# Kernel optimization log

Hardware: AMD Instinct MI355X
Metric: run time of the kernel (lower is better)

Reference implementation:

```python
import jax, jax.numpy as jnp
import numpy as np

K = 8        # number of nearest neighbors (idw default)
POWER = 2    # inverse-distance power (idw default)
EPS = 1e-8


def setup_inputs() -> dict:
    key = jax.random.key(0)
    kq, kr, kf = jax.random.split(key, 3)
    N, M = 32768, 16384
    # scale coords so points are spread out like real LiDAR scenes
    query_points = jax.random.normal(kq, (N, 3), dtype=jnp.float32) * 10.0
    ref_points = jax.random.normal(kr, (M, 3), dtype=jnp.float32) * 10.0
    ref_flow = jax.random.normal(kf, (M, 3), dtype=jnp.float32)
    return {"query_points": query_points, "ref_points": ref_points, "ref_flow": ref_flow}


def reference(query_points, ref_points, ref_flow):
    # cdist: Euclidean distance [N, M] via (q-r)^2 = |q|^2 + |r|^2 - 2 q.r
    q2 = jnp.sum(query_points * query_points, axis=-1, keepdims=True)      # [N,1]
    r2 = jnp.sum(ref_points * ref_points, axis=-1)                          # [M]
    d2 = q2 + r2 - 2.0 * (query_points @ ref_points.T)                      # [N,M]
    dist = jnp.sqrt(jnp.maximum(d2, 0.0))
    # k smallest distances == top_k of negated distances
    neg_knn, knn_idx = jax.lax.top_k(-dist, K)                               # [N,K]
    knn_dist = -neg_knn
    # inverse-distance weights: 1 / (d^power + eps), normalized over k
    weights = 1.0 / (knn_dist ** POWER + EPS)
    weights = weights / jnp.sum(weights, axis=1, keepdims=True)
    knn_flow = ref_flow[knn_idx]                                             # [N,K,3]
    return jnp.sum(weights[..., None] * knn_flow, axis=1)                    # [N,3]
```

## Files before the change

kernel.cpp:

```cpp
#include <hip/hip_runtime.h>

#define KNN    8
#define BLOCK  256
#define TILE   2048
#define GD     32
#define NC     (GD*GD*GD)
#define EPSW   1e-8f
#define BIGF   3.4e38f

__device__ __forceinline__ void insert8(float d2, int j, float bd[KNN], int bi[KNN]) {
    if (d2 < bd[0]) {
        bd[0] = d2; bi[0] = j;
#pragma unroll
        for (int t = 0; t < KNN - 1; t++) {
            if (bd[t] < bd[t + 1]) {
                float td = bd[t]; bd[t] = bd[t + 1]; bd[t + 1] = td;
                int   ti = bi[t]; bi[t] = bi[t + 1]; bi[t + 1] = ti;
            }
        }
    }
}

__device__ __forceinline__ void ced(float& a, int& ai, float& b, int& bi) {
    if (a < b) { float t = a; a = b; b = t; int ti = ai; ai = bi; bi = ti; }
}
__device__ __forceinline__ void sort8_desc(float d[KNN], int ix[KNN]) {
    ced(d[0],ix[0],d[4],ix[4]); ced(d[1],ix[1],d[5],ix[5]);
    ced(d[2],ix[2],d[6],ix[6]); ced(d[3],ix[3],d[7],ix[7]);
    ced(d[0],ix[0],d[2],ix[2]); ced(d[1],ix[1],d[3],ix[3]);
    ced(d[4],ix[4],d[6],ix[6]); ced(d[5],ix[5],d[7],ix[7]);
    ced(d[0],ix[0],d[1],ix[1]); ced(d[2],ix[2],d[3],ix[3]);
    ced(d[4],ix[4],d[5],ix[5]); ced(d[6],ix[6],d[7],ix[7]);
}
__device__ __forceinline__ void merge_lists(float bd[KNN], int bi[KNN], int mask, bool sort_after) {
    float pd[KNN]; int pi[KNN];
#pragma unroll
    for (int j = 0; j < KNN; j++) { pd[j] = __shfl_xor(bd[j], mask); pi[j] = __shfl_xor(bi[j], mask); }
#pragma unroll
    for (int j = 0; j < KNN; j++) {
        if (pd[KNN - 1 - j] < bd[j]) { bd[j] = pd[KNN - 1 - j]; bi[j] = pi[KNN - 1 - j]; }
    }
    if (sort_after) sort8_desc(bd, bi);
}
__device__ __forceinline__ float merged_thr4(const float bd[KNN]) {
    float c[KNN], p[KNN];
#pragma unroll
    for (int j = 0; j < KNN; j++) c[j] = bd[j];
#pragma unroll
    for (int j = 0; j < KNN; j++) p[j] = __shfl_xor(c[j], 1);
#pragma unroll
    for (int j = 0; j < KNN; j++) c[j] = fminf(c[j], p[KNN - 1 - j]);
    {
        float mx, mn;
        mx = fmaxf(c[0],c[4]); mn = fminf(c[0],c[4]); c[0]=mx; c[4]=mn;
        mx = fmaxf(c[1],c[5]); mn = fminf(c[1],c[5]); c[1]=mx; c[5]=mn;
        mx = fmaxf(c[2],c[6]); mn = fminf(c[2],c[6]); c[2]=mx; c[6]=mn;
        mx = fmaxf(c[3],c[7]); mn = fminf(c[3],c[7]); c[3]=mx; c[7]=mn;
        mx = fmaxf(c[0],c[2]); mn = fminf(c[0],c[2]); c[0]=mx; c[2]=mn;
        mx = fmaxf(c[1],c[3]); mn = fminf(c[1],c[3]); c[1]=mx; c[3]=mn;
        mx = fmaxf(c[4],c[6]); mn = fminf(c[4],c[6]); c[4]=mx; c[6]=mn;
        mx = fmaxf(c[5],c[7]); mn = fminf(c[5],c[7]); c[5]=mx; c[7]=mn;
        mx = fmaxf(c[0],c[1]); mn = fminf(c[0],c[1]); c[0]=mx; c[1]=mn;
        mx = fmaxf(c[2],c[3]); mn = fminf(c[2],c[3]); c[2]=mx; c[3]=mn;
        mx = fmaxf(c[4],c[5]); mn = fminf(c[4],c[5]); c[4]=mx; c[5]=mn;
        mx = fmaxf(c[6],c[7]); mn = fminf(c[6],c[7]); c[6]=mx; c[7]=mn;
    }
#pragma unroll
    for (int j = 0; j < KNN; j++) p[j] = __shfl_xor(c[j], 2);
#pragma unroll
    for (int j = 0; j < KNN; j++) c[j] = fminf(c[j], p[KNN - 1 - j]);
    float m = c[0];
#pragma unroll
    for (int j = 1; j < KNN; j++) m = fmaxf(m, c[j]);
    return m;
}

__device__ __forceinline__ unsigned fenc(float f) {
    unsigned u = __float_as_uint(f);
    return (u & 0x80000000u) ? ~u : (u | 0x80000000u);
}
__device__ __forceinline__ float fdec(unsigned e) {
    unsigned u = (e & 0x80000000u) ? (e ^ 0x80000000u) : ~e;
    return __uint_as_float(u);
}

__device__ __forceinline__ void load_bb(const unsigned* __restrict__ bbw,
                                        float mn[3], float inv[3], float& hmin) {
    hmin = BIGF;
#pragma unroll
    for (int a = 0; a < 3; a++) {
        float lo = fdec(bbw[a]), hi = -fdec(bbw[3 + a]);
        float w = fmaxf(hi - lo, 1e-9f);
        mn[a] = lo;
        inv[a] = (float)GD / w;
        hmin = fminf(hmin, w / (float)GD);
    }
}

__device__ __forceinline__ int cell_clamp(int c) {
    return c < 0 ? 0 : (c > GD - 1 ? GD - 1 : c);
}


__global__ __launch_bounds__(256) void bbox_zero(const float* __restrict__ r, int M,
                                                 unsigned* __restrict__ bbw,
                                                 int* __restrict__ zbase, int zcount) {
    int idx = blockIdx.x * 256 + threadIdx.x;
    for (int j = idx; j < zcount; j += gridDim.x * 256) zbase[j] = 0;
    float mn0 = BIGF, mn1 = BIGF, mn2 = BIGF;
    float mx0 = -BIGF, mx1 = -BIGF, mx2 = -BIGF;
    for (int j = idx; j < M; j += gridDim.x * 256) {
        float x = r[3 * j], y = r[3 * j + 1], z = r[3 * j + 2];
        mn0 = fminf(mn0, x); mx0 = fmaxf(mx0, x);
        mn1 = fminf(mn1, y); mx1 = fmaxf(mx1, y);
        mn2 = fminf(mn2, z); mx2 = fmaxf(mx2, z);
    }
#pragma unroll
    for (int o = 32; o > 0; o >>= 1) {
        mn0 = fminf(mn0, __shfl_xor(mn0, o));
        mn1 = fminf(mn1, __shfl_xor(mn1, o));
        mn2 = fminf(mn2, __shfl_xor(mn2, o));
        mx0 = fmaxf(mx0, __shfl_xor(mx0, o));
        mx1 = fmaxf(mx1, __shfl_xor(mx1, o));
        mx2 = fmaxf(mx2, __shfl_xor(mx2, o));
    }
    if ((threadIdx.x & 63) == 0) {
        atomicMin(bbw + 0, fenc(mn0)); atomicMin(bbw + 1, fenc(mn1)); atomicMin(bbw + 2, fenc(mn2));
        atomicMin(bbw + 3, fenc(-mx0)); atomicMin(bbw + 4, fenc(-mx1)); atomicMin(bbw + 5, fenc(-mx2));
    }
}

__global__ __launch_bounds__(256) void hist2(const float* __restrict__ r,
                                             const float* __restrict__ q,
                                             int M, int N, const unsigned* __restrict__ bbw,
                                             int* __restrict__ rcid, int* __restrict__ qcid,
                                             int* __restrict__ rcnt, int* __restrict__ qcnt) {
    float mn[3], inv[3], hmin;
    load_bb(bbw, mn, inv, hmin);
    int i = blockIdx.x * 256 + threadIdx.x;
    if (i < M) {
        int cx = cell_clamp((int)((r[3 * i]     - mn[0]) * inv[0]));
        int cy = cell_clamp((int)((r[3 * i + 1] - mn[1]) * inv[1]));
        int cz = cell_clamp((int)((r[3 * i + 2] - mn[2]) * inv[2]));
        int cid = (cz * GD + cy) * GD + cx;
        rcid[i] = cid;
        atomicAdd(rcnt + cid, 1);
    } else if (i < M + N) {
        int j = i - M;
        int cx = cell_clamp((int)((q[3 * j]     - mn[0]) * inv[0]));
        int cy = cell_clamp((int)((q[3 * j + 1] - mn[1]) * inv[1]));
        int cz = cell_clamp((int)((q[3 * j + 2] - mn[2]) * inv[2]));
        int cid = (cz * GD + cy) * GD + cx;
        qcid[j] = cid;
        atomicAdd(qcnt + cid, 1);
    }
}

__global__ __launch_bounds__(1024) void scan2(int* __restrict__ rcnt, int* __restrict__ rstart,
                                              int* __restrict__ qcnt, int* __restrict__ qstart) {
    int* cnt = (blockIdx.x == 0) ? rcnt : qcnt;
    int* st  = (blockIdx.x == 0) ? rstart : qstart;
    __shared__ int part[1024];
    int t = threadIdx.x;
    int base = t * 32;
    int s = 0;
#pragma unroll
    for (int k = 0; k < 32; k++) s += cnt[base + k];
    part[t] = s;
    __syncthreads();
    for (int off = 1; off < 1024; off <<= 1) {
        int v = (t >= off) ? part[t - off] : 0;
        __syncthreads();
        part[t] += v;
        __syncthreads();
    }
    int run = part[t] - s;
#pragma unroll
    for (int k = 0; k < 32; k++) {
        int c = cnt[base + k];
        st[base + k] = run;
        cnt[base + k] = run;
        run += c;
    }
    if (t == 1023) st[NC] = run;
}

__global__ __launch_bounds__(256) void scatter2(const float* __restrict__ r, int M, int N,
                                                const int* __restrict__ rcid,
                                                const int* __restrict__ qcid,
                                                int* __restrict__ rcur, int* __restrict__ qcur,
                                                float4* __restrict__ rps, int* __restrict__ sidx,
                                                int* __restrict__ qorder) {
    int i = blockIdx.x * 256 + threadIdx.x;
    if (i < M) {
        int pos = atomicAdd(rcur + rcid[i], 1);
        float x = r[3 * i], y = r[3 * i + 1], z = r[3 * i + 2];
        rps[pos] = make_float4(x, y, z, x * x + y * y + z * z);
        sidx[pos] = i;
    } else if (i < M + N) {
        int j = i - M;
        int pos = atomicAdd(qcur + qcid[j], 1);
        qorder[pos] = j;
    }
}

__device__ __forceinline__ void scan_shell(
    int R, int cx, int cy, int cz, int sub,
    const float4* __restrict__ rps, const int* __restrict__ rstart,
    float qx, float qy, float qz, float q2,
    float bd[KNN], int bi[KNN], float& thr) {
    for (int dz = -R; dz <= R; ++dz) {
        int z = cz + dz;
        if ((unsigned)z >= GD) continue;
        for (int dy = -R; dy <= R; ++dy) {
            int y = cy + dy;
            if ((unsigned)y >= GD) continue;
            int rowb = (z * GD + y) * GD;
            if (dz == -R || dz == R || dy == -R || dy == R) {
                int x0 = max(cx - R, 0), x1 = min(cx + R, GD - 1);
                int s = rstart[rowb + x0], e = rstart[rowb + x1 + 1];
                for (int ii = s + sub; ii < e; ii += 4) {
                    float4 p = rps[ii];
                    float d2 = (q2 + p.w) - 2.0f * (qx * p.x + qy * p.y + qz * p.z);
                    if (d2 < thr) { insert8(d2, ii, bd, bi); thr = bd[0]; }
                }
            } else {
                int xl = cx - R, xr = cx + R;
                if (xl >= 0) {
                    int s = rstart[rowb + xl], e = rstart[rowb + xl + 1];
                    for (int ii = s + sub; ii < e; ii += 4) {
                        float4 p = rps[ii];
                        float d2 = (q2 + p.w) - 2.0f * (qx * p.x + qy * p.y + qz * p.z);
                        if (d2 < thr) { insert8(d2, ii, bd, bi); thr = bd[0]; }
                    }
                }
                if (xr < GD) {
                    int s = rstart[rowb + xr], e = rstart[rowb + xr + 1];
                    for (int ii = s + sub; ii < e; ii += 4) {
                        float4 p = rps[ii];
                        float d2 = (q2 + p.w) - 2.0f * (qx * p.x + qy * p.y + qz * p.z);
                        if (d2 < thr) { insert8(d2, ii, bd, bi); thr = bd[0]; }
                    }
                }
            }
        }
    }
}

__global__ __launch_bounds__(256) void knn_pass1(
    const float4* __restrict__ rps, const int* __restrict__ rstart,
    const int* __restrict__ qorder, const float* __restrict__ q,
    const int* __restrict__ sidx, const float* __restrict__ f,
    const unsigned* __restrict__ bbw, float* __restrict__ out,
    int* __restrict__ pend, int* __restrict__ pcnt, int N) {
    int t = blockIdx.x * 256 + threadIdx.x;
    int g = t >> 2;
    int sub = t & 3;
    if (g >= N) return;
    int qi = qorder[g];
    float qx = q[3 * qi], qy = q[3 * qi + 1], qz = q[3 * qi + 2];
    float q2 = qx * qx + qy * qy + qz * qz;
    float mn[3], inv[3], hmin;
    load_bb(bbw, mn, inv, hmin);
    int cx = cell_clamp((int)((qx - mn[0]) * inv[0]));
    int cy = cell_clamp((int)((qy - mn[1]) * inv[1]));
    int cz = cell_clamp((int)((qz - mn[2]) * inv[2]));

    float bd[KNN]; int bi[KNN];
#pragma unroll
    for (int k = 0; k < KNN; k++) { bd[k] = BIGF; bi[k] = 0; }
    float thr = BIGF;

    int rs[9], re[9];
#pragma unroll
    for (int dz = -1; dz <= 1; dz++) {
#pragma unroll
        for (int dy = -1; dy <= 1; dy++) {
            int k = (dz + 1) * 3 + (dy + 1);
            int z = cz + dz, y = cy + dy;
            if ((unsigned)z >= GD || (unsigned)y >= GD) { rs[k] = 0; re[k] = 0; }
            else {
                int rowb = (z * GD + y) * GD;
                int x0 = max(cx - 1, 0), x1 = min(cx + 1, GD - 1);
                rs[k] = rstart[rowb + x0]; re[k] = rstart[rowb + x1 + 1];
            }
        }
    }
#pragma unroll
    for (int k = 0; k < 9; k++) {
        for (int ii = rs[k] + sub; ii < re[k]; ii += 4) {
            float4 p = rps[ii];
            float d2 = (q2 + p.w) - 2.0f * (qx * p.x + qy * p.y + qz * p.z);
            if (d2 < thr) { insert8(d2, ii, bd, bi); thr = bd[0]; }
        }
    }
    float mthr = merged_thr4(bd);
    thr = fminf(thr, mthr);
    bool done = (mthr <= hmin * hmin);

    if (!done) {
        scan_shell(2, cx, cy, cz, sub, rps, rstart, qx, qy, qz, q2, bd, bi, thr);
        mthr = merged_thr4(bd);
        thr = fminf(thr, mthr);
        done = (mthr <= 4.0f * hmin * hmin);
    }
    if (!done) {
        scan_shell(3, cx, cy, cz, sub, rps, rstart, qx, qy, qz, q2, bd, bi, thr);
        mthr = merged_thr4(bd);
        done = (mthr <= 9.0f * hmin * hmin);
    }

    if (!done) {
        if (sub == 0) { int pos = atomicAdd(pcnt, 1); pend[pos] = qi; }
        return;
    }

    merge_lists(bd, bi, 1, true);
    merge_lists(bd, bi, 2, false);
    if (sub == 0) {
        float wsum = 0.f, ox = 0.f, oy = 0.f, oz = 0.f;
#pragma unroll
        for (int k = 0; k < KNN; k++) {
            float w = 1.0f / (fmaxf(bd[k], 0.0f) + EPSW);
            int j = sidx[bi[k]];
            wsum += w;
            ox += w * f[3 * j];
            oy += w * f[3 * j + 1];
            oz += w * f[3 * j + 2];
        }
        float invw = 1.0f / wsum;
        out[3 * qi]     = ox * invw;
        out[3 * qi + 1] = oy * invw;
        out[3 * qi + 2] = oz * invw;
    }
}

__global__ __launch_bounds__(256) void knn_pass2(
    const float4* __restrict__ rps, const int* __restrict__ pend,
    const int* __restrict__ pcnt, const float* __restrict__ q,
    const int* __restrict__ sidx, const float* __restrict__ f,
    float* __restrict__ out, int M) {
    __shared__ float sd[4][KNN];
    __shared__ int   si[4][KNN];
    int tid = threadIdx.x;
    int lane = tid & 63, wv = tid >> 6;
    int cnt = *pcnt;
    for (int w = blockIdx.x; w < cnt; w += gridDim.x) {
        int qi = pend[w];
        float qx = q[3 * qi], qy = q[3 * qi + 1], qz = q[3 * qi + 2];
        float q2 = qx * qx + qy * qy + qz * qz;
        float bd[KNN]; int bi[KNN];
#pragma unroll
        for (int k = 0; k < KNN; k++) { bd[k] = BIGF; bi[k] = 0; }
        float thr = BIGF;
        int i = tid;
        for (; i + 1792 < M; i += 2048) {
            float4 p0 = rps[i];
            float4 p1 = rps[i + 256];
            float4 p2 = rps[i + 512];
            float4 p3 = rps[i + 768];
            float4 p4 = rps[i + 1024];
            float4 p5 = rps[i + 1280];
            float4 p6 = rps[i + 1536];
            float4 p7 = rps[i + 1792];
            float d0 = (q2 + p0.w) - 2.0f * (qx * p0.x + qy * p0.y + qz * p0.z);
            float d1 = (q2 + p1.w) - 2.0f * (qx * p1.x + qy * p1.y + qz * p1.z);
            float d2 = (q2 + p2.w) - 2.0f * (qx * p2.x + qy * p2.y + qz * p2.z);
            float d3 = (q2 + p3.w) - 2.0f * (qx * p3.x + qy * p3.y + qz * p3.z);
            float d4 = (q2 + p4.w) - 2.0f * (qx * p4.x + qy * p4.y + qz * p4.z);
            float d5 = (q2 + p5.w) - 2.0f * (qx * p5.x + qy * p5.y + qz * p5.z);
            float d6 = (q2 + p6.w) - 2.0f * (qx * p6.x + qy * p6.y + qz * p6.z);
            float d7 = (q2 + p7.w) - 2.0f * (qx * p7.x + qy * p7.y + qz * p7.z);
            if (d0 < thr) { insert8(d0, i,        bd, bi); thr = bd[0]; }
            if (d1 < thr) { insert8(d1, i + 256,  bd, bi); thr = bd[0]; }
            if (d2 < thr) { insert8(d2, i + 512,  bd, bi); thr = bd[0]; }
            if (d3 < thr) { insert8(d3, i + 768,  bd, bi); thr = bd[0]; }
            if (d4 < thr) { insert8(d4, i + 1024, bd, bi); thr = bd[0]; }
            if (d5 < thr) { insert8(d5, i + 1280, bd, bi); thr = bd[0]; }
            if (d6 < thr) { insert8(d6, i + 1536, bd, bi); thr = bd[0]; }
            if (d7 < thr) { insert8(d7, i + 1792, bd, bi); thr = bd[0]; }
        }
        for (; i < M; i += 256) {
            float4 p = rps[i];
            float d2 = (q2 + p.w) - 2.0f * (qx * p.x + qy * p.y + qz * p.z);
            if (d2 < thr) { insert8(d2, i, bd, bi); thr = bd[0]; }
        }
        merge_lists(bd, bi, 1, true);
        merge_lists(bd, bi, 2, true);
        merge_lists(bd, bi, 4, true);
        merge_lists(bd, bi, 8, true);
        merge_lists(bd, bi, 16, true);
        merge_lists(bd, bi, 32, true);
        if (lane == 0) {
#pragma unroll
            for (int k = 0; k < KNN; k++) { sd[wv][k] = bd[k]; si[wv][k] = bi[k]; }
        }
        __syncthreads();
        if (tid == 0) {
            for (int v = 1; v < 4; v++) {
#pragma unroll
                for (int k = 0; k < KNN; k++) insert8(sd[v][k], si[v][k], bd, bi);
            }
            float wsum = 0.f, ox = 0.f, oy = 0.f, oz = 0.f;
#pragma unroll
            for (int k = 0; k < KNN; k++) {
                float wgt = 1.0f / (fmaxf(bd[k], 0.0f) + EPSW);
                int j = sidx[bi[k]];
                wsum += wgt;
                ox += wgt * f[3 * j];
                oy += wgt * f[3 * j + 1];
                oz += wgt * f[3 * j + 2];
            }
            float invw = 1.0f / wsum;
            out[3 * qi]     = ox * invw;
            out[3 * qi + 1] = oy * invw;
            out[3 * qi + 2] = oz * invw;
        }
        __syncthreads();
    }
}

__global__ __launch_bounds__(BLOCK) void knn_fused(
    const float* __restrict__ q, const float* __restrict__ r,
    const float* __restrict__ f, float* __restrict__ out, int N, int M) {
    __shared__ float4 lds[TILE];
    int qi = blockIdx.x * BLOCK + threadIdx.x;
    float qx = 0.f, qy = 0.f, qz = 0.f, q2 = 0.f;
    if (qi < N) {
        qx = q[3 * qi]; qy = q[3 * qi + 1]; qz = q[3 * qi + 2];
        q2 = qx * qx + qy * qy + qz * qz;
    }
    float bd[KNN]; int bi[KNN];
#pragma unroll
    for (int k = 0; k < KNN; k++) { bd[k] = BIGF; bi[k] = 0; }
    for (int tb = 0; tb < M; tb += TILE) {
        int cnt = min(TILE, M - tb);
        for (int i = threadIdx.x; i < cnt; i += BLOCK) {
            int j = tb + i;
            float rx = r[3 * j], ry = r[3 * j + 1], rz = r[3 * j + 2];
            lds[i] = make_float4(rx, ry, rz, rx * rx + ry * ry + rz * rz);
        }
        __syncthreads();
        for (int i = 0; i < cnt; i++) {
            float4 p = lds[i];
            float d2 = (q2 + p.w) - 2.0f * (qx * p.x + qy * p.y + qz * p.z);
            insert8(d2, tb + i, bd, bi);
        }
        __syncthreads();
    }
    if (qi < N) {
        float wsum = 0.f, ox = 0.f, oy = 0.f, oz = 0.f;
#pragma unroll
        for (int k = 0; k < KNN; k++) {
            float w = 1.0f / (fmaxf(bd[k], 0.0f) + EPSW);
            int j = bi[k];
            ox += w * f[3 * j];
            oy += w * f[3 * j + 1];
            oz += w * f[3 * j + 2];
        }
        float inv = 1.0f / wsum;
        out[3 * qi]     = ox * inv;
        out[3 * qi + 1] = oy * inv;
        out[3 * qi + 2] = oz * inv;
    }
}

extern "C" void kernel_launch(void* const* d_in, const int* in_sizes, int n_in,
                              void* d_out, int out_size, void* d_ws, size_t ws_size,
                              hipStream_t stream) {
    const float* q = (const float*)d_in[0];
    const float* r = (const float*)d_in[1];
    const float* f = (const float*)d_in[2];
    float* out = (float*)d_out;
    int N = in_sizes[0] / 3;
    int M = in_sizes[1] / 3;

    size_t off = 0;
    auto take = [&](size_t b) { size_t o = off; off += (b + 255) & ~(size_t)255; return o; };
    size_t o_rps  = take((size_t)M * 16);
    size_t o_sidx = take((size_t)M * 4);
    size_t o_rcid = take((size_t)M * 4);
    size_t o_qcid = take((size_t)N * 4);
    size_t o_qord = take((size_t)N * 4);
    size_t o_rst  = take((size_t)(NC + 1) * 4);
    size_t o_qst  = take((size_t)(NC + 1) * 4);
    size_t o_rcur = take((size_t)NC * 4);
    size_t o_qcur = take((size_t)NC * 4);
    size_t o_pcnt = take(4);
    size_t o_pend = take((size_t)N * 4);
    size_t o_bb   = take(64);

    int grid_x = (N + BLOCK - 1) / BLOCK;
    if (off <= ws_size) {
        char* w = (char*)d_ws;
        float4* rps   = (float4*)(w + o_rps);
        int* sidx     = (int*)(w + o_sidx);
        int* rcid     = (int*)(w + o_rcid);
        int* qcid     = (int*)(w + o_qcid);
        int* qorder   = (int*)(w + o_qord);
        int* rstart   = (int*)(w + o_rst);
        int* qstart   = (int*)(w + o_qst);
        int* rcur     = (int*)(w + o_rcur);
        int* qcur     = (int*)(w + o_qcur);
        int* pcnt     = (int*)(w + o_pcnt);
        int* pend     = (int*)(w + o_pend);
        unsigned* bbw = (unsigned*)(w + o_bb);

        hipMemsetAsync(w + o_bb, 0xFF, 24, stream);

        int zcount = (int)((o_pcnt + 4 - o_rcur) / 4);
        int g_all = (M + N + 255) / 256;
        bbox_zero<<<64, 256, 0, stream>>>(r, M, bbw, rcur, zcount);
        hist2<<<g_all, 256, 0, stream>>>(r, q, M, N, bbw, rcid, qcid, rcur, qcur);
        scan2<<<2, 1024, 0, stream>>>(rcur, rstart, qcur, qstart);
        scatter2<<<g_all, 256, 0, stream>>>(r, M, N, rcid, qcid, rcur, qcur, rps, sidx, qorder);
        int g_p1 = (int)(((size_t)N * 4 + 255) / 256);
        knn_pass1<<<g_p1, 256, 0, stream>>>(rps, rstart, qorder, q, sidx, f, bbw, out,
                                            pend, pcnt, N);
        knn_pass2<<<512, 256, 0, stream>>>(rps, pend, pcnt, q, sidx, f, out, M);
    } else {
        knn_fused<<<grid_x, BLOCK, 0, stream>>>(q, r, f, out, N, M);
    }
}
```

Baseline: 202.5 us.

## Use eight lanes per query and split outer shells by cell row segment

```diff
diff --git a/kernel.cpp b/kernel.cpp
--- a/kernel.cpp
+++ b/kernel.cpp
@@ -5,6 +5,7 @@
 #define TILE   2048
 #define GD     32
 #define NC     (GD*GD*GD)
+#define LPQ    8
 #define EPSW   1e-8f
 #define BIGF   3.4e38f
 
@@ -32,6 +33,21 @@
     ced(d[0],ix[0],d[1],ix[1]); ced(d[2],ix[2],d[3],ix[3]);
     ced(d[4],ix[4],d[5],ix[5]); ced(d[6],ix[6],d[7],ix[7]);
 }
+__device__ __forceinline__ void sort8_desc_np(float c[KNN]) {
+    float mx, mn;
+    mx = fmaxf(c[0],c[4]); mn = fminf(c[0],c[4]); c[0]=mx; c[4]=mn;
+    mx = fmaxf(c[1],c[5]); mn = fminf(c[1],c[5]); c[1]=mx; c[5]=mn;
+    mx = fmaxf(c[2],c[6]); mn = fminf(c[2],c[6]); c[2]=mx; c[6]=mn;
+    mx = fmaxf(c[3],c[7]); mn = fminf(c[3],c[7]); c[3]=mx; c[7]=mn;
+    mx = fmaxf(c[0],c[2]); mn = fminf(c[0],c[2]); c[0]=mx; c[2]=mn;
+    mx = fmaxf(c[1],c[3]); mn = fminf(c[1],c[3]); c[1]=mx; c[3]=mn;
+    mx = fmaxf(c[4],c[6]); mn = fminf(c[4],c[6]); c[4]=mx; c[6]=mn;
+    mx = fmaxf(c[5],c[7]); mn = fminf(c[5],c[7]); c[5]=mx; c[7]=mn;
+    mx = fmaxf(c[0],c[1]); mn = fminf(c[0],c[1]); c[0]=mx; c[1]=mn;
+    mx = fmaxf(c[2],c[3]); mn = fminf(c[2],c[3]); c[2]=mx; c[3]=mn;
+    mx = fmaxf(c[4],c[5]); mn = fminf(c[4],c[5]); c[4]=mx; c[5]=mn;
+    mx = fmaxf(c[6],c[7]); mn = fminf(c[6],c[7]); c[6]=mx; c[7]=mn;
+}
 __device__ __forceinline__ void merge_lists(float bd[KNN], int bi[KNN], int mask, bool sort_after) {
     float pd[KNN]; int pi[KNN];
 #pragma unroll
@@ -42,7 +58,7 @@
     }
     if (sort_after) sort8_desc(bd, bi);
 }
-__device__ __forceinline__ float merged_thr4(const float bd[KNN]) {
+__device__ __forceinline__ float merged_thr8(const float bd[KNN]) {
     float c[KNN], p[KNN];
 #pragma unroll
     for (int j = 0; j < KNN; j++) c[j] = bd[j];
@@ -50,23 +66,14 @@
     for (int j = 0; j < KNN; j++) p[j] = __shfl_xor(c[j], 1);
 #pragma unroll
     for (int j = 0; j < KNN; j++) c[j] = fminf(c[j], p[KNN - 1 - j]);
-    {
-        float mx, mn;
-        mx = fmaxf(c[0],c[4]); mn = fminf(c[0],c[4]); c[0]=mx; c[4]=mn;
-        mx = fmaxf(c[1],c[5]); mn = fminf(c[1],c[5]); c[1]=mx; c[5]=mn;
-        mx = fmaxf(c[2],c[6]); mn = fminf(c[2],c[6]); c[2]=mx; c[6]=mn;
-        mx = fmaxf(c[3],c[7]); mn = fminf(c[3],c[7]); c[3]=mx; c[7]=mn;
-        mx = fmaxf(c[0],c[2]); mn = fminf(c[0],c[2]); c[0]=mx; c[2]=mn;
-        mx = fmaxf(c[1],c[3]); mn = fminf(c[1],c[3]); c[1]=mx; c[3]=mn;
-        mx = fmaxf(c[4],c[6]); mn = fminf(c[4],c[6]); c[4]=mx; c[6]=mn;
-        mx = fmaxf(c[5],c[7]); mn = fminf(c[5],c[7]); c[5]=mx; c[7]=mn;
-        mx = fmaxf(c[0],c[1]); mn = fminf(c[0],c[1]); c[0]=mx; c[1]=mn;
-        mx = fmaxf(c[2],c[3]); mn = fminf(c[2],c[3]); c[2]=mx; c[3]=mn;
-        mx = fmaxf(c[4],c[5]); mn = fminf(c[4],c[5]); c[4]=mx; c[5]=mn;
-        mx = fmaxf(c[6],c[7]); mn = fminf(c[6],c[7]); c[6]=mx; c[7]=mn;
-    }
+    sort8_desc_np(c);
 #pragma unroll
     for (int j = 0; j < KNN; j++) p[j] = __shfl_xor(c[j], 2);
+#pragma unroll
+    for (int j = 0; j < KNN; j++) c[j] = fminf(c[j], p[KNN - 1 - j]);
+    sort8_desc_np(c);
+#pragma unroll
+    for (int j = 0; j < KNN; j++) p[j] = __shfl_xor(c[j], 4);
 #pragma unroll
     for (int j = 0; j < KNN; j++) c[j] = fminf(c[j], p[KNN - 1 - j]);
     float m = c[0];
@@ -204,39 +211,42 @@
     }
 }
 
-__device__ __forceinline__ void scan_shell(
+__device__ __forceinline__ void scan_shell_seg(
     int R, int cx, int cy, int cz, int sub,
     const float4* __restrict__ rps, const int* __restrict__ rstart,
     float qx, float qy, float qz, float q2,
     float bd[KNN], int bi[KNN], float& thr) {
+    int seg = 0;
     for (int dz = -R; dz <= R; ++dz) {
         int z = cz + dz;
-        if ((unsigned)z >= GD) continue;
+        bool zok = ((unsigned)z < GD);
         for (int dy = -R; dy <= R; ++dy) {
             int y = cy + dy;
-            if ((unsigned)y >= GD) continue;
+            bool yok = ((unsigned)y < GD);
             int rowb = (z * GD + y) * GD;
             if (dz == -R || dz == R || dy == -R || dy == R) {
-                int x0 = max(cx - R, 0), x1 = min(cx + R, GD - 1);
-                int s = rstart[rowb + x0], e = rstart[rowb + x1 + 1];
-                for (int ii = s + sub; ii < e; ii += 4) {
-                    float4 p = rps[ii];
-                    float d2 = (q2 + p.w) - 2.0f * (qx * p.x + qy * p.y + qz * p.z);
-                    if (d2 < thr) { insert8(d2, ii, bd, bi); thr = bd[0]; }
-                }
-            } else {
-                int xl = cx - R, xr = cx + R;
-                if (xl >= 0) {
-                    int s = rstart[rowb + xl], e = rstart[rowb + xl + 1];
-                    for (int ii = s + sub; ii < e; ii += 4) {
+                if ((seg++ & (LPQ - 1)) == sub && zok && yok) {
+                    int x0 = max(cx - R, 0), x1 = min(cx + R, GD - 1);
+                    int s = rstart[rowb + x0], e = rstart[rowb + x1 + 1];
+                    for (int ii = s; ii < e; ++ii) {
                         float4 p = rps[ii];
                         float d2 = (q2 + p.w) - 2.0f * (qx * p.x + qy * p.y + qz * p.z);
                         if (d2 < thr) { insert8(d2, ii, bd, bi); thr = bd[0]; }
                     }
                 }
-                if (xr < GD) {
+            } else {
+                int xl = cx - R, xr = cx + R;
+                if ((seg++ & (LPQ - 1)) == sub && zok && yok && xl >= 0) {
+                    int s = rstart[rowb + xl], e = rstart[rowb + xl + 1];
+                    for (int ii = s; ii < e; ++ii) {
+                        float4 p = rps[ii];
+                        float d2 = (q2 + p.w) - 2.0f * (qx * p.x + qy * p.y + qz * p.z);
+                        if (d2 < thr) { insert8(d2, ii, bd, bi); thr = bd[0]; }
+                    }
+                }
+                if ((seg++ & (LPQ - 1)) == sub && zok && yok && xr < GD) {
                     int s = rstart[rowb + xr], e = rstart[rowb + xr + 1];
-                    for (int ii = s + sub; ii < e; ii += 4) {
+                    for (int ii = s; ii < e; ++ii) {
                         float4 p = rps[ii];
                         float d2 = (q2 + p.w) - 2.0f * (qx * p.x + qy * p.y + qz * p.z);
                         if (d2 < thr) { insert8(d2, ii, bd, bi); thr = bd[0]; }
@@ -254,8 +264,8 @@
     const unsigned* __restrict__ bbw, float* __restrict__ out,
     int* __restrict__ pend, int* __restrict__ pcnt, int N) {
     int t = blockIdx.x * 256 + threadIdx.x;
-    int g = t >> 2;
-    int sub = t & 3;
+    int g = t >> 3;
+    int sub = t & (LPQ - 1);
     if (g >= N) return;
     int qi = qorder[g];
     float qx = q[3 * qi], qy = q[3 * qi + 1], qz = q[3 * qi + 2];
@@ -288,25 +298,25 @@
     }
 #pragma unroll
     for (int k = 0; k < 9; k++) {
-        for (int ii = rs[k] + sub; ii < re[k]; ii += 4) {
+        for (int ii = rs[k] + sub; ii < re[k]; ii += LPQ) {
             float4 p = rps[ii];
             float d2 = (q2 + p.w) - 2.0f * (qx * p.x + qy * p.y + qz * p.z);
             if (d2 < thr) { insert8(d2, ii, bd, bi); thr = bd[0]; }
         }
     }
-    float mthr = merged_thr4(bd);
+    float mthr = merged_thr8(bd);
     thr = fminf(thr, mthr);
     bool done = (mthr <= hmin * hmin);
 
     if (!done) {
-        scan_shell(2, cx, cy, cz, sub, rps, rstart, qx, qy, qz, q2, bd, bi, thr);
-        mthr = merged_thr4(bd);
+        scan_shell_seg(2, cx, cy, cz, sub, rps, rstart, qx, qy, qz, q2, bd, bi, thr);
+        mthr = merged_thr8(bd);
         thr = fminf(thr, mthr);
         done = (mthr <= 4.0f * hmin * hmin);
     }
     if (!done) {
-        scan_shell(3, cx, cy, cz, sub, rps, rstart, qx, qy, qz, q2, bd, bi, thr);
-        mthr = merged_thr4(bd);
+        scan_shell_seg(3, cx, cy, cz, sub, rps, rstart, qx, qy, qz, q2, bd, bi, thr);
+        mthr = merged_thr8(bd);
         done = (mthr <= 9.0f * hmin * hmin);
     }
 
@@ -316,7 +326,8 @@
     }
 
     merge_lists(bd, bi, 1, true);
-    merge_lists(bd, bi, 2, false);
+    merge_lists(bd, bi, 2, true);
+    merge_lists(bd, bi, 4, false);
     if (sub == 0) {
         float wsum = 0.f, ox = 0.f, oy = 0.f, oz = 0.f;
 #pragma unroll
@@ -514,7 +525,7 @@
         hist2<<<g_all, 256, 0, stream>>>(r, q, M, N, bbw, rcid, qcid, rcur, qcur);
         scan2<<<2, 1024, 0, stream>>>(rcur, rstart, qcur, qstart);
         scatter2<<<g_all, 256, 0, stream>>>(r, M, N, rcid, qcid, rcur, qcur, rps, sidx, qorder);
-        int g_p1 = (int)(((size_t)N * 4 + 255) / 256);
+        int g_p1 = (int)(((size_t)N * LPQ + 255) / 256);
         knn_pass1<<<g_p1, 256, 0, stream>>>(rps, rstart, qorder, q, sidx, f, bbw, out,
                                             pend, pcnt, N);
         knn_pass2<<<512, 256, 0, stream>>>(rps, pend, pcnt, q, sidx, f, out, M);
```

Result: slower. 232.7 us (+15.0%).
